# Kernel tuning notes

Hardware: AMD Instinct MI355X
Metric: run time of the kernel (lower is better)

## Reference

```python
import jax, jax.numpy as jnp
import numpy as np

VOCAB, D_MODEL, NUM_NODES = 32000, 512, 64
BATCH, SEQ = 8, 256
LN_EPS = 1e-5


def setup_inputs() -> dict:
    key = jax.random.key(0)
    ks = jax.random.split(key, 10)
    d, n, v = D_MODEL, NUM_NODES, VOCAB
    lim_g = 1.0 / np.sqrt(2 * d)  # nn.Linear default init bound
    lim_h = 1.0 / np.sqrt(d)
    return {
        "idx": jax.random.randint(ks[0], (BATCH, SEQ), 0, v),
        "embedding": jax.random.normal(ks[1], (v, d), dtype=jnp.float32),
        "manifold_nodes": jax.random.normal(ks[2], (n, d), dtype=jnp.float32) * 0.02,
        "Wg": jax.random.uniform(ks[3], (2 * d, d), jnp.float32, -lim_g, lim_g),
        "bg": jax.random.uniform(ks[4], (d,), jnp.float32, -lim_g, lim_g),
        "Wu": jax.random.uniform(ks[5], (2 * d, d), jnp.float32, -lim_g, lim_g),
        "bu": jax.random.uniform(ks[6], (d,), jnp.float32, -lim_g, lim_g),
        "ln_w": jnp.ones((d,), jnp.float32),
        "ln_b": jnp.zeros((d,), jnp.float32),
        "Wh": jax.random.uniform(ks[7], (d, v), jnp.float32, -lim_h, lim_h),
        "bh": jax.random.uniform(ks[8], (v,), jnp.float32, -lim_h, lim_h),
    }


def _layernorm(x, w, b):
    mu = jnp.mean(x, axis=-1, keepdims=True)
    var = jnp.mean(jnp.square(x - mu), axis=-1, keepdims=True)
    return (x - mu) * jax.lax.rsqrt(var + LN_EPS) * w + b


def reference(idx, embedding, manifold_nodes, Wg, bg, Wu, bu, ln_w, ln_b, Wh, bh):
    B, S = idx.shape
    x = embedding[idx]                                   # [B,S,D]
    nodes0 = jnp.broadcast_to(manifold_nodes[None], (B,) + manifold_nodes.shape)  # [B,N,D]

    def step(nodes, x_t):
        # x_t: [B,D] -> broadcast to each node
        feats = jnp.broadcast_to(x_t[:, None, :], nodes.shape)    # [B,N,D]
        combined = jnp.concatenate([feats, nodes], axis=-1)       # [B,N,2D]
        gate = jax.nn.sigmoid(combined @ Wg + bg)                 # [B,N,D]
        cand = jnp.tanh(combined @ Wu + bu)                       # [B,N,D]
        nodes = gate * cand + (1.0 - gate) * nodes
        consensus = jnp.mean(nodes, axis=1)                       # [B,D]
        return nodes, consensus

    _, consensus_seq = jax.lax.scan(step, nodes0, jnp.swapaxes(x, 0, 1))  # [S,B,D]
    consensus = jnp.swapaxes(consensus_seq, 0, 1)                 # [B,S,D]
    logits = _layernorm(consensus, ln_w, ln_b) @ Wh + bh          # [B,S,V]
    return logits
```

## Files before the change

### kernel.cpp

```cpp
#include <hip/hip_runtime.h>


#define NBATCH 8
#define SEQ    256
#define DM     512
#define VOCAB  32000
#define NNODES 64
#define MROWS  2048
#define KT     16

typedef __attribute__((ext_vector_type(8))) short s8v;
typedef __attribute__((ext_vector_type(4))) float f4v;

#define OFF_XFRAG  0u
#define OFF_BPKTOP 2097152u
#define OFF_BPKREC 3145728u
#define OFF_WHPK   4194304u
#define OFF_XGU    36962304u
#define OFF_PART   45350912u
#define OFF_NORM   62128128u
#define OFF_XBUF   0u
#define OFF_CNT    1048576u

__device__ __forceinline__ short f2bf(float f) {
  unsigned u = __builtin_bit_cast(unsigned, f);
  u += 0x7fffu + ((u >> 16) & 1u);
  return (short)(u >> 16);
}
__device__ __forceinline__ float fsig(float x) {
  float e = __builtin_amdgcn_exp2f(-1.4426950408889634f * x);
  return __builtin_amdgcn_rcpf(1.0f + e);
}
__device__ __forceinline__ float ftanh(float x) {
  float xc = fminf(fmaxf(x, -15.0f), 15.0f);
  float e = __builtin_amdgcn_exp2f(2.8853900817779268f * xc);
  return (e - 1.0f) * __builtin_amdgcn_rcpf(e + 1.0f);
}

__global__ __launch_bounds__(256) void k_packw(const float* __restrict__ Wg,
                                               const float* __restrict__ Wu,
                                               short* __restrict__ top,
                                               short* __restrict__ rec) {
  int t = blockIdx.x * 256 + threadIdx.x;
  int l = t & 63, kt = (t >> 6) & 15, nt = (t >> 10) & 31;
  int ub = (t >> 15) & 1, tb = (t >> 16) & 1;
  const float* src = ub ? Wu : Wg;
  int row0 = tb * 512 + kt * 32 + ((l >> 4) << 3);
  int col  = nt * 16 + (l & 15);
  short* dst = tb ? rec : top;
  int base = (((ub * 32 + nt) * KT + kt) * 64 + l) * 8;
#pragma unroll
  for (int j = 0; j < 8; ++j) dst[base + j] = f2bf(src[(row0 + j) * 512 + col]);
}

__global__ __launch_bounds__(256) void k_packwh(const float* __restrict__ Wh,
                                                short* __restrict__ whpk) {
  int t = blockIdx.x * 256 + threadIdx.x;
  int l = t & 63, kt = (t >> 6) & 15, nt = t >> 10;
  int row0 = kt * 32 + ((l >> 4) << 3);
  int col  = nt * 16 + (l & 15);
  int base = ((nt * KT + kt) * 64 + l) * 8;
#pragma unroll
  for (int j = 0; j < 8; ++j) whpk[base + j] = f2bf(Wh[(row0 + j) * VOCAB + col]);
}

__global__ __launch_bounds__(256) void k_gather(const int* __restrict__ idx,
                                                const float* __restrict__ emb,
                                                short* __restrict__ xfrag) {
  int t = blockIdx.x * 256 + threadIdx.x;
  int l = t & 63, kt = (t >> 6) & 15, mt = t >> 10;
  int m = mt * 16 + (l & 15);
  int tok = idx[m];
  const float* e = emb + (long)tok * DM + kt * 32 + ((l >> 4) << 3);
  int base = ((mt * KT + kt) * 64 + l) * 8;
#pragma unroll
  for (int j = 0; j < 8; ++j) xfrag[base + j] = f2bf(e[j]);
}

__global__ __launch_bounds__(256) void k_xgemm(const short* __restrict__ xfrag,
                                               const short* __restrict__ bpk,
                                               const float* __restrict__ bg,
                                               const float* __restrict__ bu,
                                               float* __restrict__ xgu) {
  int tid = threadIdx.x, l = tid & 63, w = tid >> 6;
  int mtb = blockIdx.x;
  int nt  = blockIdx.y * 4 + w;
  f4v acc[4];
#pragma unroll
  for (int mi = 0; mi < 4; ++mi) acc[mi] = 0;
  for (int kt = 0; kt < KT; ++kt) {
    s8v bf = *(const s8v*)(bpk + ((nt * KT + kt) * 64 + l) * 8);
#pragma unroll
    for (int mi = 0; mi < 4; ++mi) {
      s8v a = *(const s8v*)(xfrag + (((mtb * 4 + mi) * KT + kt) * 64 + l) * 8);
      acc[mi] = __builtin_amdgcn_mfma_f32_16x16x32_bf16(a, bf, acc[mi], 0, 0, 0);
    }
  }
  int n = nt * 16 + (l & 15);
  float bias = (n < 512) ? bg[n] : bu[n - 512];
#pragma unroll
  for (int mi = 0; mi < 4; ++mi)
#pragma unroll
    for (int r = 0; r < 4; ++r) {
      int m = (mtb * 4 + mi) * 16 + ((l >> 4) << 2) + r;
      xgu[m * 1024 + n] = acc[mi][r] + bias;
    }
}

__global__ __launch_bounds__(256) void k_zero(unsigned* __restrict__ cnt) {
  cnt[blockIdx.x * 256 + threadIdx.x] = 0u;
}

__global__ __launch_bounds__(256, 1) void k_recur8(const short* __restrict__ bpk,
                                                   const float* __restrict__ xgu,
                                                   const float* __restrict__ mn,
                                                   float* __restrict__ part,
                                                   short* __restrict__ xbuf,
                                                   unsigned* __restrict__ cnt) {
  __shared__ short hfrag[KT * 64 * 8];
  const int tid = threadIdx.x;
  const int l = tid & 63, w = tid >> 6;
  const int lm = l & 15, lq = l >> 4;
  const int g = blockIdx.x >> 3;
  const int oct = blockIdx.x & 7;
  const int bat = g >> 2, nb = g & 3;
  unsigned* cg = cnt + g * 32;

  s8v wgr[KT], wur[KT];
  const int ng = 4 * oct + w;
#pragma unroll
  for (int kt = 0; kt < KT; ++kt) {
    wgr[kt] = *(const s8v*)(bpk + ((ng * KT + kt) * 64 + l) * 8);
    wur[kt] = *(const s8v*)(bpk + (((32 + ng) * KT + kt) * 64 + l) * 8);
  }

  const int col = 64 * oct + 16 * w + lm;
  float hm[4];
#pragma unroll
  for (int r = 0; r < 4; ++r)
    hm[r] = mn[(nb * 16 + lq * 4 + r) * DM + col];

#pragma unroll
  for (int q = 0; q < 4; ++q) {
    int idx = q * 256 + tid;
    int kt = idx >> 6, ln = idx & 63;
    int node = nb * 16 + (ln & 15);
    const float* src = mn + node * DM + kt * 32 + ((ln >> 4) << 3);
    short tmp[8];
#pragma unroll
    for (int j = 0; j < 8; ++j) tmp[j] = f2bf(src[j]);
    *(s8v*)(hfrag + (kt * 64 + ln) * 8) = *(s8v*)tmp;
  }
  __syncthreads();

  float xg = xgu[(bat * SEQ) * 1024 + col];
  float xu = xgu[(bat * SEQ) * 1024 + 512 + col];

  for (int t = 0; t < SEQ; ++t) {
    f4v accg = 0, accu = 0;
#pragma unroll
    for (int kt = 0; kt < KT; ++kt) {
      s8v a = *(const s8v*)(hfrag + (kt * 64 + l) * 8);
      accg = __builtin_amdgcn_mfma_f32_16x16x32_bf16(a, wgr[kt], accg, 0, 0, 0);
      accu = __builtin_amdgcn_mfma_f32_16x16x32_bf16(a, wur[kt], accu, 0, 0, 0);
    }
    float ps = 0.0f;
#pragma unroll
    for (int r = 0; r < 4; ++r) {
      float gg = fsig(accg[r] + xg);
      float cc = ftanh(accu[r] + xu);
      float h = gg * cc + (1.0f - gg) * hm[r];
      hm[r] = h;
      ps += h;
    }
    ps += __shfl_xor(ps, 16);
    ps += __shfl_xor(ps, 32);
    if (l < 16)
      part[(((bat * 4 + nb) * SEQ + t) * DM) + col] = ps;

    if (t < SEQ - 1) {
      const int par = (t + 1) & 1;
      unsigned* xw = (unsigned*)xbuf + (par * 32 + g) * 4096;
#pragma unroll
      for (int r = 0; r < 4; ++r) {
        float pr = __shfl_xor(hm[r], 1);
        if (!(lm & 1)) {
          unsigned pv = (unsigned)(unsigned short)f2bf(hm[r])
                      | ((unsigned)(unsigned short)f2bf(pr) << 16);
          int node = lq * 4 + r;
          __hip_atomic_store(xw + ((node * 512 + col) >> 1), pv,
                             __ATOMIC_RELAXED, __HIP_MEMORY_SCOPE_AGENT);
        }
      }
      const float* xrowN = xgu + (bat * SEQ + t + 1) * 1024;
      float xgN = xrowN[col], xuN = xrowN[512 + col];
      __syncthreads();
      if (tid == 0) {
        __hip_atomic_fetch_add(cg, 1u, __ATOMIC_RELAXED,
                               __HIP_MEMORY_SCOPE_AGENT);
        const unsigned tgt = 8u * (unsigned)(t + 1);
        int spins = 0;
        while (__hip_atomic_load(cg, __ATOMIC_RELAXED,
                                 __HIP_MEMORY_SCOPE_AGENT) < tgt) {
          __builtin_amdgcn_s_sleep(2);
          if (++spins > 4096) break;
        }
      }
      __syncthreads();
      const unsigned* xr = (const unsigned*)xbuf + (par * 32 + g) * 4096;
#pragma unroll
      for (int q = 0; q < 4; ++q) {
        int idx = q * 256 + tid;
        int kt = idx >> 6, ln = idx & 63;
        int o32 = ((ln & 15) * 512 + kt * 32 + ((ln >> 4) << 3)) >> 1;
        unsigned d0 = __hip_atomic_load(xr + o32 + 0, __ATOMIC_RELAXED,
                                        __HIP_MEMORY_SCOPE_AGENT);
        unsigned d1 = __hip_atomic_load(xr + o32 + 1, __ATOMIC_RELAXED,
                                        __HIP_MEMORY_SCOPE_AGENT);
        unsigned d2 = __hip_atomic_load(xr + o32 + 2, __ATOMIC_RELAXED,
                                        __HIP_MEMORY_SCOPE_AGENT);
        unsigned d3 = __hip_atomic_load(xr + o32 + 3, __ATOMIC_RELAXED,
                                        __HIP_MEMORY_SCOPE_AGENT);
        union { unsigned u[4]; s8v v; } c;
        c.u[0] = d0; c.u[1] = d1; c.u[2] = d2; c.u[3] = d3;
        *(s8v*)(hfrag + (kt * 64 + ln) * 8) = c.v;
      }
      xg = xgN;
      xu = xuN;
      __syncthreads();
    }
  }
}

__global__ __launch_bounds__(1024) void k_ln(const float* __restrict__ part,
                                             const float* __restrict__ lnw,
                                             const float* __restrict__ lnb,
                                             short* __restrict__ nfrag) {
  __shared__ short tile[16 * DM];
  int tid = threadIdx.x, w = tid >> 6, l = tid & 63;
  int bI = blockIdx.x;
  int m = bI * 16 + w;
  int bat = m >> 8, t = m & 255;
  const float* p0 = part + ((bat * 4) * SEQ + t) * DM;
  float vx[8];
#pragma unroll
  for (int j = 0; j < 8; ++j) {
    int d = l * 8 + j;
    vx[j] = (p0[d] + p0[d + 131072] + p0[d + 262144] + p0[d + 393216]) * (1.0f / 64.0f);
  }
  float s = 0;
#pragma unroll
  for (int j = 0; j < 8; ++j) s += vx[j];
  for (int msk = 1; msk < 64; msk <<= 1) s += __shfl_xor(s, msk);
  float mean = s * (1.0f / 512.0f);
  float q = 0;
#pragma unroll
  for (int j = 0; j < 8; ++j) { float d = vx[j] - mean; q += d * d; }
  for (int msk = 1; msk < 64; msk <<= 1) q += __shfl_xor(q, msk);
  float rs = rsqrtf(q * (1.0f / 512.0f) + 1e-5f);
#pragma unroll
  for (int j = 0; j < 8; ++j) {
    int d = l * 8 + j;
    tile[w * DM + d] = f2bf((vx[j] - mean) * rs * lnw[d] + lnb[d]);
  }
  __syncthreads();
  s8v val = *(const s8v*)(&tile[(l & 15) * DM + w * 32 + ((l >> 4) << 3)]);
  *(s8v*)(nfrag + ((bI * KT + w) * 64 + l) * 8) = val;
}

__global__ __launch_bounds__(512) void k_logits(const short* __restrict__ nfrag,
                                                const short* __restrict__ whpk,
                                                const float* __restrict__ bh,
                                                float* __restrict__ out) {
  int tid = threadIdx.x, l = tid & 63, w = tid >> 6;
  int wm = w >> 2, wn = w & 3;
  int ntb = blockIdx.x;
  int mtb = blockIdx.y;
  f4v acc[8][4];
#pragma unroll
  for (int mi = 0; mi < 8; ++mi)
#pragma unroll
    for (int ni = 0; ni < 4; ++ni) acc[mi][ni] = 0;
  for (int kt = 0; kt < KT; ++kt) {
    s8v bf[4];
#pragma unroll
    for (int ni = 0; ni < 4; ++ni)
      bf[ni] = *(const s8v*)(whpk + (((ntb * 16 + wn * 4 + ni) * KT + kt) * 64 + l) * 8);
#pragma unroll
    for (int mi = 0; mi < 8; ++mi) {
      s8v a = *(const s8v*)(nfrag + (((mtb * 16 + wm * 8 + mi) * KT + kt) * 64 + l) * 8);
#pragma unroll
      for (int ni = 0; ni < 4; ++ni)
        acc[mi][ni] = __builtin_amdgcn_mfma_f32_16x16x32_bf16(a, bf[ni], acc[mi][ni], 0, 0, 0);
    }
  }
#pragma unroll
  for (int ni = 0; ni < 4; ++ni) {
    int n = (ntb * 16 + wn * 4 + ni) * 16 + (l & 15);
    float bias = bh[n];
#pragma unroll
    for (int mi = 0; mi < 8; ++mi) {
      int mrow = (mtb * 16 + wm * 8 + mi) * 16 + ((l >> 4) << 2);
#pragma unroll
      for (int r = 0; r < 4; ++r)
        out[(long)(mrow + r) * VOCAB + n] = acc[mi][ni][r] + bias;
    }
  }
}

extern "C" void kernel_launch(void* const* d_in, const int* in_sizes, int n_in,
                              void* d_out, int out_size, void* d_ws, size_t ws_size,
                              hipStream_t stream) {
  (void)in_sizes; (void)n_in; (void)out_size; (void)ws_size;
  const int*   idx = (const int*)  d_in[0];
  const float* emb = (const float*)d_in[1];
  const float* mn  = (const float*)d_in[2];
  const float* Wg  = (const float*)d_in[3];
  const float* bg  = (const float*)d_in[4];
  const float* Wu  = (const float*)d_in[5];
  const float* bu  = (const float*)d_in[6];
  const float* lnw = (const float*)d_in[7];
  const float* lnb = (const float*)d_in[8];
  const float* Wh  = (const float*)d_in[9];
  const float* bh  = (const float*)d_in[10];
  float* out = (float*)d_out;
  char* ws = (char*)d_ws;
  short* xfrag  = (short*)(ws + OFF_XFRAG);
  short* bpktop = (short*)(ws + OFF_BPKTOP);
  short* bpkrec = (short*)(ws + OFF_BPKREC);
  short* whpk   = (short*)(ws + OFF_WHPK);
  float* xgu    = (float*)(ws + OFF_XGU);
  float* part   = (float*)(ws + OFF_PART);
  short* nfrag  = (short*)(ws + OFF_NORM);
  short* xbuf   = (short*)(ws + OFF_XBUF);
  unsigned* cnt = (unsigned*)(ws + OFF_CNT);

  k_packw <<<dim3(512),      dim3(256),  0, stream>>>(Wg, Wu, bpktop, bpkrec);
  k_packwh<<<dim3(8000),     dim3(256),  0, stream>>>(Wh, whpk);
  k_gather<<<dim3(512),      dim3(256),  0, stream>>>(idx, emb, xfrag);
  k_xgemm <<<dim3(32, 16),   dim3(256),  0, stream>>>(xfrag, bpktop, bg, bu, xgu);
  k_zero  <<<dim3(4),        dim3(256),  0, stream>>>(cnt);
  k_recur8<<<dim3(256),      dim3(256),  0, stream>>>(bpkrec, xgu, mn, part, xbuf, cnt);
  k_ln    <<<dim3(128),      dim3(1024), 0, stream>>>(part, lnw, lnb, nfrag);
  k_logits<<<dim3(125, 8),   dim3(512),  0, stream>>>(nfrag, whpk, bh, out);
}
```

Measured before the change: 1.489 ms.

## Replace atomic counter barrier with per-block flags and fragment-layout exchange buffer

The recurrence kernel's cross-block barrier uses per-block release-store flags polled in parallel by one wavefront, replacing the single contended fetch_add counter polled by one thread. The exchange buffer now holds hidden state directly in MFMA fragment order, so each thread reloads LDS with contiguous 64-bit atomic loads instead of scattered 32-bit gathers. Block-to-group mapping is interleaved across the grid, and empty asm statements pin the weight registers across iterations. The aim is a shorter per-timestep synchronization and exchange latency on the serial critical path. The risks are a wrong fragment index mapping and the cost of reading eight flags per step.

```diff
diff --git a/kernel.cpp b/kernel.cpp
--- a/kernel.cpp
+++ b/kernel.cpp
@@ -20,7 +20,7 @@
 #define OFF_PART   45350912u
 #define OFF_NORM   62128128u
 #define OFF_XBUF   0u
-#define OFF_CNT    1048576u
+#define OFF_FLAGS  1048576u
 
 __device__ __forceinline__ short f2bf(float f) {
   unsigned u = __builtin_bit_cast(unsigned, f);
@@ -107,8 +107,8 @@
     }
 }
 
-__global__ __launch_bounds__(256) void k_zero(unsigned* __restrict__ cnt) {
-  cnt[blockIdx.x * 256 + threadIdx.x] = 0u;
+__global__ __launch_bounds__(256) void k_zero(unsigned* __restrict__ flags) {
+  flags[blockIdx.x * 256 + threadIdx.x] = 0u;
 }
 
 __global__ __launch_bounds__(256, 1) void k_recur8(const short* __restrict__ bpk,
@@ -116,15 +116,15 @@
                                                    const float* __restrict__ mn,
                                                    float* __restrict__ part,
                                                    short* __restrict__ xbuf,
-                                                   unsigned* __restrict__ cnt) {
+                                                   unsigned* __restrict__ flags) {
   __shared__ short hfrag[KT * 64 * 8];
   const int tid = threadIdx.x;
   const int l = tid & 63, w = tid >> 6;
   const int lm = l & 15, lq = l >> 4;
-  const int g = blockIdx.x >> 3;
-  const int oct = blockIdx.x & 7;
+  const int bid = blockIdx.x;
+  const int g = bid & 31;
+  const int oct = bid >> 5;
   const int bat = g >> 2, nb = g & 3;
-  unsigned* cg = cnt + g * 32;
 
   s8v wgr[KT], wur[KT];
   const int ng = 4 * oct + w;
@@ -149,18 +149,29 @@
     short tmp[8];
 #pragma unroll
     for (int j = 0; j < 8; ++j) tmp[j] = f2bf(src[j]);
-    *(s8v*)(hfrag + (kt * 64 + ln) * 8) = *(s8v*)tmp;
+    *(s8v*)(&hfrag[(kt * 64 + ln) * 8]) = *(s8v*)tmp;
   }
   __syncthreads();
+
+  const int kt_out = 2 * oct + (w >> 1);
+  const int kk = 16 * (w & 1) + lm;
 
   float xg = xgu[(bat * SEQ) * 1024 + col];
   float xu = xgu[(bat * SEQ) * 1024 + 512 + col];
 
   for (int t = 0; t < SEQ; ++t) {
+    asm volatile("" : "+v"(wgr[0]), "+v"(wgr[1]), "+v"(wgr[2]), "+v"(wgr[3]),
+                      "+v"(wgr[4]), "+v"(wgr[5]), "+v"(wgr[6]), "+v"(wgr[7]));
+    asm volatile("" : "+v"(wgr[8]), "+v"(wgr[9]), "+v"(wgr[10]), "+v"(wgr[11]),
+                      "+v"(wgr[12]), "+v"(wgr[13]), "+v"(wgr[14]), "+v"(wgr[15]));
+    asm volatile("" : "+v"(wur[0]), "+v"(wur[1]), "+v"(wur[2]), "+v"(wur[3]),
+                      "+v"(wur[4]), "+v"(wur[5]), "+v"(wur[6]), "+v"(wur[7]));
+    asm volatile("" : "+v"(wur[8]), "+v"(wur[9]), "+v"(wur[10]), "+v"(wur[11]),
+                      "+v"(wur[12]), "+v"(wur[13]), "+v"(wur[14]), "+v"(wur[15]));
     f4v accg = 0, accu = 0;
 #pragma unroll
     for (int kt = 0; kt < KT; ++kt) {
-      s8v a = *(const s8v*)(hfrag + (kt * 64 + l) * 8);
+      s8v a = *(const s8v*)(&hfrag[(kt * 64 + l) * 8]);
       accg = __builtin_amdgcn_mfma_f32_16x16x32_bf16(a, wgr[kt], accg, 0, 0, 0);
       accu = __builtin_amdgcn_mfma_f32_16x16x32_bf16(a, wur[kt], accu, 0, 0, 0);
     }
@@ -187,44 +198,37 @@
         if (!(lm & 1)) {
           unsigned pv = (unsigned)(unsigned short)f2bf(hm[r])
                       | ((unsigned)(unsigned short)f2bf(pr) << 16);
-          int node = lq * 4 + r;
-          __hip_atomic_store(xw + ((node * 512 + col) >> 1), pv,
+          int ln = ((kk >> 3) << 4) | (lq * 4 + r);
+          __hip_atomic_store(xw + (kt_out * 64 + ln) * 4 + ((kk & 7) >> 1), pv,
                              __ATOMIC_RELAXED, __HIP_MEMORY_SCOPE_AGENT);
         }
       }
-      const float* xrowN = xgu + (bat * SEQ + t + 1) * 1024;
-      float xgN = xrowN[col], xuN = xrowN[512 + col];
+      const float* xrN = xgu + (bat * SEQ + t + 1) * 1024;
+      float xgN = xrN[col], xuN = xrN[512 + col];
       __syncthreads();
-      if (tid == 0) {
-        __hip_atomic_fetch_add(cg, 1u, __ATOMIC_RELAXED,
-                               __HIP_MEMORY_SCOPE_AGENT);
-        const unsigned tgt = 8u * (unsigned)(t + 1);
+      if (tid == 0)
+        __hip_atomic_store(flags + (g * 8 + oct) * 16, (unsigned)(t + 1),
+                           __ATOMIC_RELEASE, __HIP_MEMORY_SCOPE_AGENT);
+      if (w == 0) {
+        int o = l & 7;
         int spins = 0;
-        while (__hip_atomic_load(cg, __ATOMIC_RELAXED,
-                                 __HIP_MEMORY_SCOPE_AGENT) < tgt) {
-          __builtin_amdgcn_s_sleep(2);
-          if (++spins > 4096) break;
+        while (__hip_atomic_load(flags + (g * 8 + o) * 16, __ATOMIC_RELAXED,
+                                 __HIP_MEMORY_SCOPE_AGENT) < (unsigned)(t + 1)) {
+          __builtin_amdgcn_s_sleep(1);
+          if (++spins > 65536) break;
         }
       }
       __syncthreads();
-      const unsigned* xr = (const unsigned*)xbuf + (par * 32 + g) * 4096;
-#pragma unroll
-      for (int q = 0; q < 4; ++q) {
-        int idx = q * 256 + tid;
-        int kt = idx >> 6, ln = idx & 63;
-        int o32 = ((ln & 15) * 512 + kt * 32 + ((ln >> 4) << 3)) >> 1;
-        unsigned d0 = __hip_atomic_load(xr + o32 + 0, __ATOMIC_RELAXED,
-                                        __HIP_MEMORY_SCOPE_AGENT);
-        unsigned d1 = __hip_atomic_load(xr + o32 + 1, __ATOMIC_RELAXED,
-                                        __HIP_MEMORY_SCOPE_AGENT);
-        unsigned d2 = __hip_atomic_load(xr + o32 + 2, __ATOMIC_RELAXED,
-                                        __HIP_MEMORY_SCOPE_AGENT);
-        unsigned d3 = __hip_atomic_load(xr + o32 + 3, __ATOMIC_RELAXED,
-                                        __HIP_MEMORY_SCOPE_AGENT);
-        union { unsigned u[4]; s8v v; } c;
-        c.u[0] = d0; c.u[1] = d1; c.u[2] = d2; c.u[3] = d3;
-        *(s8v*)(hfrag + (kt * 64 + ln) * 8) = c.v;
-      }
+      const unsigned long long* xr64 =
+          (const unsigned long long*)xbuf + (par * 32 + g) * 2048 + tid * 8;
+      unsigned long long v[8];
+#pragma unroll
+      for (int i = 0; i < 8; ++i)
+        v[i] = __hip_atomic_load(xr64 + i, __ATOMIC_RELAXED,
+                                 __HIP_MEMORY_SCOPE_AGENT);
+      unsigned long long* hd = (unsigned long long*)&hfrag[tid * 32];
+#pragma unroll
+      for (int i = 0; i < 8; ++i) hd[i] = v[i];
       xg = xgN;
       xu = xuN;
       __syncthreads();
@@ -333,14 +337,14 @@
   float* part   = (float*)(ws + OFF_PART);
   short* nfrag  = (short*)(ws + OFF_NORM);
   short* xbuf   = (short*)(ws + OFF_XBUF);
-  unsigned* cnt = (unsigned*)(ws + OFF_CNT);
+  unsigned* flg = (unsigned*)(ws + OFF_FLAGS);
 
   k_packw <<<dim3(512),      dim3(256),  0, stream>>>(Wg, Wu, bpktop, bpkrec);
   k_packwh<<<dim3(8000),     dim3(256),  0, stream>>>(Wh, whpk);
   k_gather<<<dim3(512),      dim3(256),  0, stream>>>(idx, emb, xfrag);
   k_xgemm <<<dim3(32, 16),   dim3(256),  0, stream>>>(xfrag, bpktop, bg, bu, xgu);
-  k_zero  <<<dim3(4),        dim3(256),  0, stream>>>(cnt);
-  k_recur8<<<dim3(256),      dim3(256),  0, stream>>>(bpkrec, xgu, mn, part, xbuf, cnt);
+  k_zero  <<<dim3(16),       dim3(256),  0, stream>>>(flg);
+  k_recur8<<<dim3(256),      dim3(256),  0, stream>>>(bpkrec, xgu, mn, part, xbuf, flg);
   k_ln    <<<dim3(128),      dim3(1024), 0, stream>>>(part, lnw, lnb, nfrag);
   k_logits<<<dim3(125, 8),   dim3(512),  0, stream>>>(nfrag, whpk, bh, out);
 }
```

After: 2.052 ms. +37.8%, slower.
